# Kernel optimization log

Hardware: AMD Instinct MI355X
Metric: run time of the kernel (lower is better)

## Reference

```python
import jax, jax.numpy as jnp
import numpy as np

N, E = 100000, 1600000
D_IN, D_H, D_OUT = 128, 128, 64


def setup_inputs() -> dict:
    key = jax.random.key(0)
    ks = jax.random.split(key, 5)
    x = jax.random.normal(ks[0], (N, D_IN), dtype=jnp.float32)
    edge_index = jax.random.randint(ks[1], (2, E), 0, N, dtype=jnp.int64)
    edge_weight = jax.random.uniform(ks[2], (E,), dtype=jnp.float32)
    W1 = jax.random.normal(ks[3], (D_IN, D_H), dtype=jnp.float32) / np.sqrt(D_IN).astype(np.float32)
    b1 = jnp.zeros((D_H,), jnp.float32)
    W2 = jax.random.normal(ks[4], (D_H, D_OUT), dtype=jnp.float32) / np.sqrt(D_H).astype(np.float32)
    b2 = jnp.zeros((D_OUT,), jnp.float32)
    return {"x": x, "edge_index": edge_index, "edge_weight": edge_weight,
            "W1": W1, "b1": b1, "W2": W2, "b2": b2}


def gcn_conv(x, row, col, ew, W, b):
    # PyG GCNConv: symmetric gcn_norm with self-loops (fill value 1.0)
    n = x.shape[0]
    deg = jax.ops.segment_sum(ew, col, num_segments=n) + 1.0  # +1 from self-loop
    dis = jax.lax.rsqrt(deg)                                   # deg^{-1/2}
    norm = dis[row] * ew * dis[col]                            # [E]
    xw = x @ W                                                 # [N, out]
    agg = jax.ops.segment_sum(norm[:, None] * xw[row], col, num_segments=n)
    agg = agg + (dis * dis)[:, None] * xw                      # self-loop messages (weight 1)
    return agg + b


def reference(x, edge_index, edge_weight, W1, b1, W2, b2):
    row, col = edge_index[0], edge_index[1]
    h = jax.nn.relu(gcn_conv(x, row, col, edge_weight, W1, b1))
    # F.dropout(training=False) is identity in eval mode
    return gcn_conv(h, row, col, edge_weight, W2, b2)
```

## Files before the change

kernel.cpp:

```cpp
#include <hip/hip_runtime.h>
#include <stdint.h>

typedef unsigned int uint32;
typedef _Float16 f16x8 __attribute__((ext_vector_type(8)));
typedef float f32x4 __attribute__((ext_vector_type(4)));


#define NPBSH 6
#define NPB 64
#define PBLK 256
#define CAP 2048

__global__ void detect_kernel(const int* __restrict__ ei, int* flag) {
    if (threadIdx.x == 0 && blockIdx.x == 0) {
        int z = 0;
        for (int i = 0; i < 16; ++i) z |= ei[2 * i + 1];
        *flag = (z == 0) ? 1 : 0;
    }
}

__global__ __launch_bounds__(512) void p1_hist(const void* __restrict__ ei, int E, int NB,
                                               int chunk, const int* __restrict__ flag,
                                               int* __restrict__ cnt_bb) {
    extern __shared__ int h[];
    const int t = threadIdx.x, blk = blockIdx.x;
    for (int i = t; i < NB; i += 512) h[i] = 0;
    __syncthreads();
    const int is64 = *flag;
    const int* e32 = (const int*)ei;
    const long long* e64 = (const long long*)ei;
    const int e0 = blk * chunk;
    const int e1 = min(e0 + chunk, E);
    for (int e = e0 + t; e < e1; e += 512) {
        int c = is64 ? (int)e64[(size_t)E + e] : e32[(size_t)E + e];
        atomicAdd(&h[c >> NPBSH], 1);
    }
    __syncthreads();
    for (int i = t; i < NB; i += 512) cnt_bb[(size_t)blk * NB + i] = h[i];
}

__global__ __launch_bounds__(PBLK) void s1_colscan(const int* __restrict__ cnt_bb,
                                                   int* __restrict__ boff_rel,
                                                   int* __restrict__ tb, int NB) {
    __shared__ int sm[PBLK];
    const int t = threadIdx.x, b = blockIdx.x;
    int v = cnt_bb[(size_t)t * NB + b];
    sm[t] = v;
    __syncthreads();
    for (int off = 1; off < PBLK; off <<= 1) {
        int u = (t >= off) ? sm[t - off] : 0;
        __syncthreads();
        sm[t] += u;
        __syncthreads();
    }
    boff_rel[(size_t)t * NB + b] = sm[t] - v;
    if (t == PBLK - 1) tb[b] = sm[PBLK - 1];
}

__global__ __launch_bounds__(1024) void scan_kernel(const int* __restrict__ cnt,
                                                    int* __restrict__ ptr, int n) {
    __shared__ int sm[1024];
    const int t = threadIdx.x;
    const int chunk = (n + 1023) / 1024;
    const int start = t * chunk;
    const int end = min(start + chunk, n);
    int s = 0;
    for (int i = start; i < end; ++i) s += cnt[i];
    sm[t] = s;
    __syncthreads();
    for (int off = 1; off < 1024; off <<= 1) {
        int v = (t >= off) ? sm[t - off] : 0;
        __syncthreads();
        sm[t] += v;
        __syncthreads();
    }
    int run = (t == 0) ? 0 : sm[t - 1];
    for (int i = start; i < end; ++i) { ptr[i] = run; run += cnt[i]; }
    if (start < n && end == n) ptr[n] = run;
}

__global__ __launch_bounds__(512) void p2_scatter(const void* __restrict__ ei,
                                                  const float* __restrict__ ew,
                                                  int E, int NB, int chunk,
                                                  const int* __restrict__ flag,
                                                  const int* __restrict__ bstart,
                                                  const int* __restrict__ boff_rel,
                                                  int2* __restrict__ bktrec,
                                                  unsigned short* __restrict__ bktc) {
    extern __shared__ int cur[];
    const int t = threadIdx.x, blk = blockIdx.x;
    for (int i = t; i < NB; i += 512)
        cur[i] = bstart[i] + boff_rel[(size_t)blk * NB + i];
    __syncthreads();
    const int is64 = *flag;
    const int* e32 = (const int*)ei;
    const long long* e64 = (const long long*)ei;
    const int e0 = blk * chunk;
    const int e1 = min(e0 + chunk, E);
    for (int e = e0 + t; e < e1; e += 512) {
        int r, c;
        if (is64) { r = (int)e64[e]; c = (int)e64[(size_t)E + e]; }
        else      { r = e32[e];      c = e32[(size_t)E + e]; }
        int b = c >> NPBSH;
        int pos = atomicAdd(&cur[b], 1);
        bktrec[pos] = make_int2(r, __float_as_int(ew[e]));
        bktc[pos] = (unsigned short)(c & (NPB - 1));
    }
}

__global__ __launch_bounds__(256) void p3_build(const int* __restrict__ bstart,
                                                const int2* __restrict__ bktrec,
                                                const unsigned short* __restrict__ bktc,
                                                int* __restrict__ ptr, int* __restrict__ rows_s,
                                                float* __restrict__ ws_s, float* __restrict__ dis,
                                                int n, int NB, int E) {
    __shared__ int inr[CAP];
    __shared__ float inw[CAP];
    __shared__ unsigned short inc[CAP];
    __shared__ int outr[CAP];
    __shared__ float outw[CAP];
    __shared__ int h[NPB], ex[NPB + 1], cu[NPB];
    const int t = threadIdx.x, b = blockIdx.x;
    const int base = bstart[b];
    const int eb = bstart[b + 1] - base;
    const int j0 = b << NPBSH;
    const int ncount = min(NPB, n - j0);
    if (t < NPB) { h[t] = 0; cu[t] = 0; }
    __syncthreads();

    if (eb <= CAP) {
        for (int i = t; i < eb; i += 256) {
            int2 rc = bktrec[base + i];
            inr[i] = rc.x;
            inw[i] = __int_as_float(rc.y);
            int cl = bktc[base + i];
            inc[i] = (unsigned short)cl;
            atomicAdd(&h[cl], 1);
        }
        __syncthreads();
        if (t == 0) {
            int run = 0;
            for (int j = 0; j < NPB; ++j) { ex[j] = run; run += h[j]; }
            ex[NPB] = run;
        }
        __syncthreads();
        for (int i = t; i < eb; i += 256) {
            int cl = inc[i];
            int d = ex[cl] + atomicAdd(&cu[cl], 1);
            outr[d] = inr[i];
            outw[d] = inw[i];
        }
        __syncthreads();
        for (int i = t; i < eb; i += 256) {
            rows_s[base + i] = outr[i];
            ws_s[base + i] = outw[i];
        }
        if (t < ncount) {
            ptr[j0 + t] = base + ex[t];
            float s = 0.f;
            for (int i = ex[t]; i < ex[t] + h[t]; ++i) s += outw[i];
            dis[j0 + t] = rsqrtf(s + 1.0f);
        }
    } else {
        for (int i = t; i < eb; i += 256) atomicAdd(&h[bktc[base + i]], 1);
        __syncthreads();
        if (t == 0) {
            int run = 0;
            for (int j = 0; j < NPB; ++j) { ex[j] = run; run += h[j]; }
            ex[NPB] = run;
        }
        __syncthreads();
        for (int i = t; i < eb; i += 256) {
            int2 rc = bktrec[base + i];
            int cl = bktc[base + i];
            int d = ex[cl] + atomicAdd(&cu[cl], 1);
            rows_s[base + d] = rc.x;
            ws_s[base + d] = __int_as_float(rc.y);
        }
        __syncthreads();
        if (t < ncount) {
            ptr[j0 + t] = base + ex[t];
            float s = 0.f;
            for (int i = base + ex[t]; i < base + ex[t] + h[t]; ++i) s += ws_s[i];
            dis[j0 + t] = rsqrtf(s + 1.0f);
        }
    }
    if (b == NB - 1 && t == 0) ptr[n] = E;
}

__global__ void fold_kernel(const int* __restrict__ rows_s, float* __restrict__ ws_s,
                            const float* __restrict__ dis, int E) {
    for (int e = blockIdx.x * blockDim.x + threadIdx.x; e < E;
         e += gridDim.x * blockDim.x)
        ws_s[e] *= dis[rows_s[e]];
}

__device__ inline uint32 pack2h(float a, float b) {
    unsigned short ua = __builtin_bit_cast(unsigned short, (_Float16)a);
    unsigned short ub = __builtin_bit_cast(unsigned short, (_Float16)b);
    return (uint32)ua | ((uint32)ub << 16);
}
__device__ inline float h2lo(uint32 g) {
    return (float)__builtin_bit_cast(_Float16, (unsigned short)(g & 0xFFFFu));
}
__device__ inline float h2hi(uint32 g) {
    return (float)__builtin_bit_cast(_Float16, (unsigned short)(g >> 16));
}

__device__ inline int kposb(int k) {
    return ((k >> 5) << 6) + (((k >> 2) & 3) << 4) + (((k >> 4) & 1) << 3) + ((k & 3) << 1);
}

template <int DOUT, bool PACKED>
__global__ __launch_bounds__(256, 2) void mgemm_kernel(const void* __restrict__ Xv,
                                                       const float* __restrict__ W,
                                                       unsigned short* __restrict__ Y,
                                                       int n) {
    constexpr int NC = DOUT / 16;
    __shared__ __align__(16) unsigned short Xl[128 * 128];
    __shared__ __align__(16) unsigned short Wl[DOUT * 128];
    const int t = threadIdx.x;
    const int row0 = blockIdx.x * 128;

    for (int i = t * 4; i < 128 * 128; i += 1024) {
        int r = i >> 7, k = i & 127;
        uint2 st;
        if (PACKED) {
            uint2 v = {0u, 0u};
            if (row0 + r < n)
                v = *(const uint2*)((const uint32*)Xv + (size_t)(row0 + r) * 64 + (k >> 1));
            st = v;
        } else {
            float4 v = {0.f, 0.f, 0.f, 0.f};
            if (row0 + r < n)
                v = *(const float4*)((const float*)Xv + (size_t)(row0 + r) * 128 + k);
            st.x = pack2h(v.x, v.y);
            st.y = pack2h(v.z, v.w);
        }
        *(uint2*)((char*)Xl + r * 256 + (kposb(k) ^ ((r & 7) << 4))) = st;
    }
    for (int i = t; i < 128 * (DOUT / 4); i += 256) {
        int k = i / (DOUT / 4);
        int c0 = (i % (DOUT / 4)) * 4;
        float4 wv = *(const float4*)(W + (size_t)k * DOUT + c0);
        float a[4] = {wv.x, wv.y, wv.z, wv.w};
        int kb = kposb(k);
#pragma unroll
        for (int j = 0; j < 4; ++j) {
            int c = c0 + j;
            *(unsigned short*)((char*)Wl + c * 256 + (kb ^ ((c & 7) << 4))) =
                __builtin_bit_cast(unsigned short, (_Float16)a[j]);
        }
    }
    __syncthreads();

    const int l = t & 63;
    const int w = t >> 6;
    const int lr = l & 15;
    const int lq = l >> 4;
    const int rbase = w * 32;
    const int swz = (lr & 7) << 4;

    f32x4 acc[2][NC];
#pragma unroll
    for (int i = 0; i < 2; ++i)
#pragma unroll
        for (int c = 0; c < NC; ++c) acc[i][c] = (f32x4){0.f, 0.f, 0.f, 0.f};

#pragma unroll
    for (int ks = 0; ks < 4; ++ks) {
        const int fo = ks * 64 + lq * 16;
        f16x8 a0 = *(const f16x8*)((const char*)Xl + (rbase + lr) * 256 + (fo ^ swz));
        f16x8 a1 = *(const f16x8*)((const char*)Xl + (rbase + 16 + lr) * 256 + (fo ^ swz));
#pragma unroll
        for (int c = 0; c < NC; ++c) {
            f16x8 b = *(const f16x8*)((const char*)Wl + (c * 16 + lr) * 256 + (fo ^ swz));
            acc[0][c] = __builtin_amdgcn_mfma_f32_16x16x32_f16(a0, b, acc[0][c], 0, 0, 0);
            acc[1][c] = __builtin_amdgcn_mfma_f32_16x16x32_f16(a1, b, acc[1][c], 0, 0, 0);
        }
    }

#pragma unroll
    for (int i = 0; i < 2; ++i) {
#pragma unroll
        for (int c = 0; c < NC; ++c) {
#pragma unroll
            for (int reg = 0; reg < 4; ++reg) {
                int row = row0 + rbase + i * 16 + lq * 4 + reg;
                if (row < n)
                    Y[(size_t)row * DOUT + c * 16 + lr] =
                        __builtin_bit_cast(unsigned short, (_Float16)acc[i][c][reg]);
            }
        }
    }
}

__global__ __launch_bounds__(256) void prop128_kernel(const uint32* __restrict__ xwb,
                                                      const float* __restrict__ dis,
                                                      const int* __restrict__ ptr,
                                                      const int* __restrict__ rows_s,
                                                      const float* __restrict__ ws_s,
                                                      const float* __restrict__ bias,
                                                      uint32* __restrict__ out, int n) {
    const int wid = threadIdx.x >> 6;
    const int lane = threadIdx.x & 63;
    const int v = blockIdx.x * 4 + wid;
    if (v >= n) return;

    const int beg = __builtin_amdgcn_readfirstlane(ptr[v]);
    const int end = __builtin_amdgcn_readfirstlane(ptr[v + 1]);
    const float dv = dis[v];

    float acc0 = 0.f, acc1 = 0.f;
    int e = beg;
    int head = (beg + 3) & ~3;
    if (head > end) head = end;
    for (; e < head; ++e) {
        int r = rows_s[e];
        float w = ws_s[e];
        uint32 g = xwb[(size_t)r * 64 + lane];
        acc0 += w * h2lo(g);
        acc1 += w * h2hi(g);
    }
#pragma unroll 2
    for (; e + 4 <= end; e += 4) {
        int4 r4 = *(const int4*)(rows_s + e);
        float4 w4 = *(const float4*)(ws_s + e);
        uint32 g0 = xwb[(size_t)r4.x * 64 + lane];
        uint32 g1 = xwb[(size_t)r4.y * 64 + lane];
        uint32 g2 = xwb[(size_t)r4.z * 64 + lane];
        uint32 g3 = xwb[(size_t)r4.w * 64 + lane];
        acc0 += w4.x * h2lo(g0); acc1 += w4.x * h2hi(g0);
        acc0 += w4.y * h2lo(g1); acc1 += w4.y * h2hi(g1);
        acc0 += w4.z * h2lo(g2); acc1 += w4.z * h2hi(g2);
        acc0 += w4.w * h2lo(g3); acc1 += w4.w * h2hi(g3);
    }
    for (; e < end; ++e) {
        int r = rows_s[e];
        float w = ws_s[e];
        uint32 g = xwb[(size_t)r * 64 + lane];
        acc0 += w * h2lo(g);
        acc1 += w * h2hi(g);
    }

    uint32 g = xwb[(size_t)v * 64 + lane];
    float r0 = dv * acc0 + dv * dv * h2lo(g) + bias[lane * 2];
    float r1 = dv * acc1 + dv * dv * h2hi(g) + bias[lane * 2 + 1];
    r0 = fmaxf(r0, 0.f);
    r1 = fmaxf(r1, 0.f);
    out[(size_t)v * 64 + lane] = pack2h(r0, r1);
}

__global__ __launch_bounds__(256) void prop64_kernel(const uint32* __restrict__ xwb,
                                                     const float* __restrict__ dis,
                                                     const int* __restrict__ ptr,
                                                     const int* __restrict__ rows_s,
                                                     const float* __restrict__ ws_s,
                                                     const float* __restrict__ bias,
                                                     float* __restrict__ out, int n) {
    const int wid = threadIdx.x >> 6;
    const int lane = threadIdx.x & 63;
    const int half = lane >> 5;
    const int dlane = lane & 31;
    const int v = blockIdx.x * 4 + wid;
    if (v >= n) return;

    const int beg = __builtin_amdgcn_readfirstlane(ptr[v]);
    const int end = __builtin_amdgcn_readfirstlane(ptr[v + 1]);
    const float dv = dis[v];

    float acc0 = 0.f, acc1 = 0.f;
    int e = beg;
    int head = (beg + 3) & ~3;
    if (head > end) head = end;
    for (; e < head; ++e) {
        int r = rows_s[e];
        float w = half ? 0.f : ws_s[e];
        uint32 g = xwb[(size_t)r * 32 + dlane];
        acc0 += w * h2lo(g);
        acc1 += w * h2hi(g);
    }
#pragma unroll 2
    for (; e + 4 <= end; e += 4) {
        int4 r4 = *(const int4*)(rows_s + e);
        float4 w4 = *(const float4*)(ws_s + e);
        int rA = half ? r4.y : r4.x;
        float wA = half ? w4.y : w4.x;
        int rB = half ? r4.w : r4.z;
        float wB = half ? w4.w : w4.z;
        uint32 gA = xwb[(size_t)rA * 32 + dlane];
        uint32 gB = xwb[(size_t)rB * 32 + dlane];
        acc0 += wA * h2lo(gA); acc1 += wA * h2hi(gA);
        acc0 += wB * h2lo(gB); acc1 += wB * h2hi(gB);
    }
    if (e + 2 <= end) {
        int2 r2 = *(const int2*)(rows_s + e);
        float2 w2 = *(const float2*)(ws_s + e);
        int r = half ? r2.y : r2.x;
        float w = half ? w2.y : w2.x;
        uint32 g = xwb[(size_t)r * 32 + dlane];
        acc0 += w * h2lo(g);
        acc1 += w * h2hi(g);
        e += 2;
    }
    if (e < end) {
        int r = rows_s[e];
        float w = half ? 0.f : ws_s[e];
        uint32 g = xwb[(size_t)r * 32 + dlane];
        acc0 += w * h2lo(g);
        acc1 += w * h2hi(g);
    }
    acc0 += __shfl_xor(acc0, 32);
    acc1 += __shfl_xor(acc1, 32);

    if (lane < 32) {
        uint32 g = xwb[(size_t)v * 32 + lane];
        float r0 = dv * acc0 + dv * dv * h2lo(g) + bias[lane * 2];
        float r1 = dv * acc1 + dv * dv * h2hi(g) + bias[lane * 2 + 1];
        float2 o = {r0, r1};
        *(float2*)(out + (size_t)v * 64 + lane * 2) = o;
    }
}

extern "C" void kernel_launch(void* const* d_in, const int* in_sizes, int n_in,
                              void* d_out, int out_size, void* d_ws, size_t ws_size,
                              hipStream_t stream) {
    const float* x  = (const float*)d_in[0];
    const void*  ei = d_in[1];
    const float* ew = (const float*)d_in[2];
    const float* W1 = (const float*)d_in[3];
    const float* b1 = (const float*)d_in[4];
    const float* W2 = (const float*)d_in[5];
    const float* b2 = (const float*)d_in[6];
    float* out = (float*)d_out;

    const int n = in_sizes[0] / 128;
    const int E = in_sizes[2];
    const int NB = (n + NPB - 1) >> NPBSH;
    const int chunk = (E + PBLK - 1) / PBLK;

    char* p = (char*)d_ws;
    size_t o = 0;
    auto alloc = [&](size_t bytes) -> void* {
        void* q = p + o;
        o += (bytes + 255) & ~(size_t)255;
        return q;
    };
    int*    flag     = (int*)alloc(4);
    int*    cnt_bb   = (int*)alloc((size_t)PBLK * NB * 4);
    int*    boff_rel = (int*)alloc((size_t)PBLK * NB * 4);
    int*    tb       = (int*)alloc((size_t)NB * 4);
    int*    bstart   = (int*)alloc(((size_t)NB + 1) * 4);
    int*    ptr      = (int*)alloc(((size_t)n + 1) * 4);
    float*  dis      = (float*)alloc((size_t)n * 4);
    int2*   bktrec   = (int2*)alloc((size_t)E * 8);
    unsigned short* bktc = (unsigned short*)alloc((size_t)E * 2 + 16);
    int*    rows_s   = (int*)alloc(((size_t)E + 8) * 4);
    float*  ws_s     = (float*)alloc(((size_t)E + 8) * 4);
    uint32* bufA     = (uint32*)alloc((size_t)n * 64 * 4);
    uint32* bufB     = (uint32*)alloc((size_t)n * 64 * 4);

    const int gblk = (n + 127) / 128;

    detect_kernel<<<1, 64, 0, stream>>>((const int*)ei, flag);
    p1_hist<<<PBLK, 512, NB * 4, stream>>>(ei, E, NB, chunk, flag, cnt_bb);
    s1_colscan<<<NB, PBLK, 0, stream>>>(cnt_bb, boff_rel, tb, NB);
    scan_kernel<<<1, 1024, 0, stream>>>(tb, bstart, NB);
    p2_scatter<<<PBLK, 512, NB * 4, stream>>>(ei, ew, E, NB, chunk, flag, bstart,
                                              boff_rel, bktrec, bktc);
    p3_build<<<NB, 256, 0, stream>>>(bstart, bktrec, bktc, ptr, rows_s, ws_s, dis, n, NB, E);
    fold_kernel<<<2048, 256, 0, stream>>>(rows_s, ws_s, dis, E);

    mgemm_kernel<128, false><<<gblk, 256, 0, stream>>>(x, W1, (unsigned short*)bufA, n);
    prop128_kernel<<<(n + 3) / 4, 256, 0, stream>>>(bufA, dis, ptr, rows_s, ws_s, b1, bufB, n);
    mgemm_kernel<64, true><<<gblk, 256, 0, stream>>>(bufB, W2, (unsigned short*)bufA, n);
    prop64_kernel<<<(n + 3) / 4, 256, 0, stream>>>(bufA, dis, ptr, rows_s, ws_s, b2, out, n);
}
```

Measured before the change: 256.6 us.

## Pack local column into row index, remap chunk blocks, deepen propagation unroll

Packs the 6-bit in-bucket column into the high bits of the row index so the separate ushort column array and its writes and reads are dropped, which cuts scatter traffic and shared memory in the build kernel. Remaps block-to-chunk assignment in the histogram and scatter kernels so consecutive block IDs handle chunks spread across the edge list. Raises the unroll of the propagation gather loops from 2 to 4 for more loads in flight. Packing relies on node indices fitting in 20 bits (N=100000), and the larger unroll raises register pressure.

```diff
diff --git a/kernel.cpp b/kernel.cpp
--- a/kernel.cpp
+++ b/kernel.cpp
@@ -19,11 +19,16 @@
     }
 }
 
+__device__ inline int chunk_map(int blk) {
+    return (blk & 7) * (PBLK / 8) + (blk >> 3);
+}
+
 __global__ __launch_bounds__(512) void p1_hist(const void* __restrict__ ei, int E, int NB,
                                                int chunk, const int* __restrict__ flag,
                                                int* __restrict__ cnt_bb) {
     extern __shared__ int h[];
-    const int t = threadIdx.x, blk = blockIdx.x;
+    const int t = threadIdx.x;
+    const int blk = chunk_map(blockIdx.x);
     for (int i = t; i < NB; i += 512) h[i] = 0;
     __syncthreads();
     const int is64 = *flag;
@@ -85,10 +90,10 @@
                                                   const int* __restrict__ flag,
                                                   const int* __restrict__ bstart,
                                                   const int* __restrict__ boff_rel,
-                                                  int2* __restrict__ bktrec,
-                                                  unsigned short* __restrict__ bktc) {
+                                                  int2* __restrict__ bktrec) {
     extern __shared__ int cur[];
-    const int t = threadIdx.x, blk = blockIdx.x;
+    const int t = threadIdx.x;
+    const int blk = chunk_map(blockIdx.x);
     for (int i = t; i < NB; i += 512)
         cur[i] = bstart[i] + boff_rel[(size_t)blk * NB + i];
     __syncthreads();
@@ -103,20 +108,17 @@
         else      { r = e32[e];      c = e32[(size_t)E + e]; }
         int b = c >> NPBSH;
         int pos = atomicAdd(&cur[b], 1);
-        bktrec[pos] = make_int2(r, __float_as_int(ew[e]));
-        bktc[pos] = (unsigned short)(c & (NPB - 1));
+        bktrec[pos] = make_int2(r | ((c & (NPB - 1)) << 20), __float_as_int(ew[e]));
     }
 }
 
 __global__ __launch_bounds__(256) void p3_build(const int* __restrict__ bstart,
                                                 const int2* __restrict__ bktrec,
-                                                const unsigned short* __restrict__ bktc,
                                                 int* __restrict__ ptr, int* __restrict__ rows_s,
                                                 float* __restrict__ ws_s, float* __restrict__ dis,
                                                 int n, int NB, int E) {
-    __shared__ int inr[CAP];
+    __shared__ int inp[CAP];
     __shared__ float inw[CAP];
-    __shared__ unsigned short inc[CAP];
     __shared__ int outr[CAP];
     __shared__ float outw[CAP];
     __shared__ int h[NPB], ex[NPB + 1], cu[NPB];
@@ -131,11 +133,9 @@
     if (eb <= CAP) {
         for (int i = t; i < eb; i += 256) {
             int2 rc = bktrec[base + i];
-            inr[i] = rc.x;
+            inp[i] = rc.x;
             inw[i] = __int_as_float(rc.y);
-            int cl = bktc[base + i];
-            inc[i] = (unsigned short)cl;
-            atomicAdd(&h[cl], 1);
+            atomicAdd(&h[(rc.x >> 20) & 63], 1);
         }
         __syncthreads();
         if (t == 0) {
@@ -145,9 +145,10 @@
         }
         __syncthreads();
         for (int i = t; i < eb; i += 256) {
-            int cl = inc[i];
+            int v = inp[i];
+            int cl = (v >> 20) & 63;
             int d = ex[cl] + atomicAdd(&cu[cl], 1);
-            outr[d] = inr[i];
+            outr[d] = v & 0xFFFFF;
             outw[d] = inw[i];
         }
         __syncthreads();
@@ -162,7 +163,7 @@
             dis[j0 + t] = rsqrtf(s + 1.0f);
         }
     } else {
-        for (int i = t; i < eb; i += 256) atomicAdd(&h[bktc[base + i]], 1);
+        for (int i = t; i < eb; i += 256) atomicAdd(&h[(bktrec[base + i].x >> 20) & 63], 1);
         __syncthreads();
         if (t == 0) {
             int run = 0;
@@ -172,9 +173,9 @@
         __syncthreads();
         for (int i = t; i < eb; i += 256) {
             int2 rc = bktrec[base + i];
-            int cl = bktc[base + i];
+            int cl = (rc.x >> 20) & 63;
             int d = ex[cl] + atomicAdd(&cu[cl], 1);
-            rows_s[base + d] = rc.x;
+            rows_s[base + d] = rc.x & 0xFFFFF;
             ws_s[base + d] = __int_as_float(rc.y);
         }
         __syncthreads();
@@ -322,7 +323,7 @@
         acc0 += w * h2lo(g);
         acc1 += w * h2hi(g);
     }
-#pragma unroll 2
+#pragma unroll 4
     for (; e + 4 <= end; e += 4) {
         int4 r4 = *(const int4*)(rows_s + e);
         float4 w4 = *(const float4*)(ws_s + e);
@@ -380,7 +381,7 @@
         acc0 += w * h2lo(g);
         acc1 += w * h2hi(g);
     }
-#pragma unroll 2
+#pragma unroll 4
     for (; e + 4 <= end; e += 4) {
         int4 r4 = *(const int4*)(rows_s + e);
         float4 w4 = *(const float4*)(ws_s + e);
@@ -454,7 +455,6 @@
     int*    ptr      = (int*)alloc(((size_t)n + 1) * 4);
     float*  dis      = (float*)alloc((size_t)n * 4);
     int2*   bktrec   = (int2*)alloc((size_t)E * 8);
-    unsigned short* bktc = (unsigned short*)alloc((size_t)E * 2 + 16);
     int*    rows_s   = (int*)alloc(((size_t)E + 8) * 4);
     float*  ws_s     = (float*)alloc(((size_t)E + 8) * 4);
     uint32* bufA     = (uint32*)alloc((size_t)n * 64 * 4);
@@ -467,8 +467,8 @@
     s1_colscan<<<NB, PBLK, 0, stream>>>(cnt_bb, boff_rel, tb, NB);
     scan_kernel<<<1, 1024, 0, stream>>>(tb, bstart, NB);
     p2_scatter<<<PBLK, 512, NB * 4, stream>>>(ei, ew, E, NB, chunk, flag, bstart,
-                                              boff_rel, bktrec, bktc);
-    p3_build<<<NB, 256, 0, stream>>>(bstart, bktrec, bktc, ptr, rows_s, ws_s, dis, n, NB, E);
+                                              boff_rel, bktrec);
+    p3_build<<<NB, 256, 0, stream>>>(bstart, bktrec, ptr, rows_s, ws_s, dis, n, NB, E);
     fold_kernel<<<2048, 256, 0, stream>>>(rows_s, ws_s, dis, E);
 
     mgemm_kernel<128, false><<<gblk, 256, 0, stream>>>(x, W1, (unsigned short*)bufA, n);
```

Result: faster. 233.4 us (-9.0%).
